# Optimization experiments

Hardware: AMD Instinct MI355X
Metric: run time of the kernel (lower is better)

The kernel has to match this reference:

```python
import jax, jax.numpy as jnp
import numpy as np

H = 256   # lstm2 hidden size
D_IN = 512  # lstm2 input size (256 fed-back out + 256 audio)
BN_EPS = 1e-5


def _lstm_cell(x, h, c, Wih, Whh, bih, bhh):
    # torch gate order: i, f, g, o
    z = x @ Wih.T + h @ Whh.T + bih + bhh  # (B, 4H)
    i, f, g, o = jnp.split(z, 4, axis=-1)
    i = jax.nn.sigmoid(i)
    f = jax.nn.sigmoid(f)
    g = jnp.tanh(g)
    o = jax.nn.sigmoid(o)
    c = f * c + i * g
    h = o * jnp.tanh(c)
    return h, c


def setup_inputs() -> dict:
    key = jax.random.key(0)
    ks = jax.random.split(key, 16)
    B, T, L = 256, 512, 16
    s = 0.05
    inp = {
        "rt": jax.random.normal(ks[0], (B, H), jnp.float32),
        "audio": jax.random.normal(ks[1], (B, T, H), jnp.float32),
        "s_rt": jax.random.normal(ks[2], (B, L, H), jnp.float32),
        # lstm2 layer 0
        "W_ih_l0": jax.random.normal(ks[3], (4 * H, D_IN), jnp.float32) * s,
        "W_hh_l0": jax.random.normal(ks[4], (4 * H, H), jnp.float32) * s,
        "b_ih_l0": jax.random.normal(ks[5], (4 * H,), jnp.float32) * s,
        "b_hh_l0": jax.random.normal(ks[6], (4 * H,), jnp.float32) * s,
        # lstm2 layer 1
        "W_ih_l1": jax.random.normal(ks[7], (4 * H, H), jnp.float32) * s,
        "W_hh_l1": jax.random.normal(ks[8], (4 * H, H), jnp.float32) * s,
        "b_ih_l1": jax.random.normal(ks[9], (4 * H,), jnp.float32) * s,
        "b_hh_l1": jax.random.normal(ks[10], (4 * H,), jnp.float32) * s,
        # rt_linear head: Linear(256,128) -> BN(128) -> ReLU -> Linear(128,6)
        "W1": jax.random.normal(ks[11], (128, H), jnp.float32) * s,
        "b1": jax.random.normal(ks[12], (128,), jnp.float32) * s,
        "gamma": jnp.ones((128,), jnp.float32),
        "beta": jnp.zeros((128,), jnp.float32),
        "W2": jax.random.normal(ks[13], (6, 128), jnp.float32) * s,
        "b2": jax.random.normal(ks[14], (6,), jnp.float32) * s,
        "max_len": 0,
    }
    return inp


def reference(rt, audio, s_rt,
              W_ih_l0, W_hh_l0, b_ih_l0, b_hh_l0,
              W_ih_l1, W_hh_l1, b_ih_l1, b_hh_l1,
              W1, b1, gamma, beta, W2, b2, max_len):
    B, T, _ = audio.shape
    prev_out = jnp.mean(s_rt, axis=1)  # (B, 256): torch.mean(s_rt, dim=1)
    h1 = c1 = h2 = c2 = jnp.zeros((B, H), audio.dtype)

    def step(carry, a_t):
        prev_out, h1, c1, h2, c2 = carry
        x = jnp.concatenate([prev_out, a_t], axis=-1)  # (B, 512)
        h1n, c1n = _lstm_cell(x, h1, c1, W_ih_l0, W_hh_l0, b_ih_l0, b_hh_l0)
        h2n, c2n = _lstm_cell(h1n, h2, c2, W_ih_l1, W_hh_l1, b_ih_l1, b_hh_l1)
        return (h2n, h1n, c1n, h2n, c2n), h2n

    audio_tm = jnp.transpose(audio, (1, 0, 2))  # (T, B, 256) time-major
    _, out_tm = jax.lax.scan(step, (prev_out, h1, c1, h2, c2), audio_tm)
    out = jnp.transpose(out_tm, (1, 0, 2)).reshape(-1, H)  # (B*T, 256)

    # rt_linear head, BatchNorm1d in training mode (batch stats)
    y = out @ W1.T + b1  # (B*T, 128)
    mu = jnp.mean(y, axis=0)
    var = jnp.var(y, axis=0)
    y = (y - mu) * jax.lax.rsqrt(var + BN_EPS) * gamma + beta
    y = jax.nn.relu(y)
    y = y @ W2.T + b2  # (B*T, 6)
    return y.reshape(B, T, -1)
```

## Files before the change

### kernel.cpp

```cpp
#include <hip/hip_runtime.h>
#include <stdint.h>

typedef unsigned int u32;
typedef unsigned short u16;
typedef unsigned long long u64;
typedef _Float16 f16;
typedef _Float16 h2_t __attribute__((ext_vector_type(2)));
typedef _Float16 f16x4 __attribute__((ext_vector_type(4)));
typedef _Float16 f16x8 __attribute__((ext_vector_type(8)));
typedef float f32x4 __attribute__((ext_vector_type(4)));
typedef float f32x16 __attribute__((ext_vector_type(16)));

#define TT 512
#define NF 128
#define NTOT (256 * TT)

#define OFF_WA0   0u
#define OFF_WA1   1572864u
#define OFF_WAH   2621440u
#define OFF_GSUM  2883584u
#define OFF_GSQ   2884096u
#define OFF_CTR   2884608u
#define OFF_GH1   2886656u
#define OFF_GH2   3017728u
#define OFF_Y     3148800u

__device__ __forceinline__ float sigf(float x) { return 1.0f / (1.0f + __expf(-x)); }
__device__ __forceinline__ float tanh_fast(float x) { return 1.0f - 2.0f / (__expf(2.0f * x) + 1.0f); }

__global__ void prep_kernel(const float* __restrict__ Wih0, const float* __restrict__ Whh0,
                            const float* __restrict__ Wih1, const float* __restrict__ Whh1,
                            const float* __restrict__ W1,
                            f16* __restrict__ WA0, f16* __restrict__ WA1, f16* __restrict__ WAH,
                            float* __restrict__ gz, u32* __restrict__ ctr) {
    int idx = blockIdx.x * 256 + threadIdx.x;
    const int n0 = 786432, n1 = 524288, n2 = 131072;
    if (idx < n0) {
        int u = idx >> 9, r9 = idx & 511;
        int lane = r9 >> 3, j = r9 & 7;
        int ks = u % 6; u /= 6;
        int wv = u & 7, w = u >> 3;
        int lr = lane & 31, h = lane >> 5;
        int r = ((lr >> 3) << 8) + 8 * w + (lr & 7);
        int seg = ks >> 1, sig = ks & 1;
        int c = 256 * seg + 32 * wv + 16 * sig + 8 * h + j;
        float v = (c < 512) ? Wih0[r * 512 + c] : Whh0[r * 256 + (c - 512)];
        WA0[idx] = (f16)v;
    } else if (idx < n0 + n1) {
        int i2 = idx - n0;
        int lane = (i2 >> 3) & 63, j = i2 & 7;
        int ks = (i2 >> 9) & 3, wv = (i2 >> 11) & 7, w = i2 >> 14;
        int lr = lane & 31, h = lane >> 5;
        int r = ((lr >> 3) << 8) + 8 * w + (lr & 7);
        int sig = ks & 1;
        int c = 32 * wv + 16 * sig + 8 * h + j;
        float v = (ks >> 1) ? Whh1[r * 256 + c] : Wih1[r * 256 + c];
        WA1[i2] = (f16)v;
    } else if (idx < n0 + n1 + n2) {
        int i2 = idx - n0 - n1;
        int u = i2 >> 9, r9 = i2 & 511;
        int lane = r9 >> 3, j = r9 & 7;
        int ks = u & 7, w = u >> 3;
        int m = lane & 15, hh = lane >> 4;
        int k = 32 * ks + 8 * hh + j;
        float v = (m < 4) ? W1[(4 * w + m) * 256 + k] : 0.f;
        WAH[i2] = (f16)v;
    } else if (idx < n0 + n1 + n2 + 256) {
        gz[idx - n0 - n1 - n2] = 0.f;
    } else if (idx < n0 + n1 + n2 + 256 + 512) {
        ctr[idx - n0 - n1 - n2 - 256] = 0u;
    }
}

#define MFMA32L(A, BP, C) (C) = __builtin_amdgcn_mfma_f32_32x32x16_f16( \
    __builtin_bit_cast(f16x8, (A)), __builtin_bit_cast(f16x8, *(const uint4*)(BP)), (C), 0, 0, 0)
#define MFMA32R(A, B, C) (C) = __builtin_amdgcn_mfma_f32_32x32x16_f16( \
    __builtin_bit_cast(f16x8, (A)), __builtin_bit_cast(f16x8, (B)), (C), 0, 0, 0)

#define ZZWR(KW, C) do { \
    f32x4 v0_ = {(C)[0], (C)[1], (C)[2], (C)[3]};    *(f32x4*)&zz[KW][n32][4 * h32] = v0_; \
    f32x4 v1_ = {(C)[4], (C)[5], (C)[6], (C)[7]};    *(f32x4*)&zz[KW][n32][8 + 4 * h32] = v1_; \
    f32x4 v2_ = {(C)[8], (C)[9], (C)[10], (C)[11]};  *(f32x4*)&zz[KW][n32][16 + 4 * h32] = v2_; \
    f32x4 v3_ = {(C)[12], (C)[13], (C)[14], (C)[15]}; *(f32x4*)&zz[KW][n32][24 + 4 * h32] = v3_; } while (0)

__global__ __launch_bounds__(512) void lstm_group_kernel(
    const float* __restrict__ audio, const float* __restrict__ s_rt,
    const uint4* __restrict__ WA0, const uint4* __restrict__ WA1, const uint4* __restrict__ WAH,
    const float* __restrict__ bih0, const float* __restrict__ bhh0,
    const float* __restrict__ bih1, const float* __restrict__ bhh1,
    const float* __restrict__ b1, u32* __restrict__ ctr,
    u64* __restrict__ gh1u, u64* __restrict__ gh2u,
    f16* __restrict__ ybuf, float* __restrict__ gsum, float* __restrict__ gsq)
{
    __shared__ f16 Xa[32][264];
    __shared__ f16 Xh2[32][264];
    __shared__ float zz[8][32][36];
    __shared__ f16 hst[32][8];
    __shared__ float bc0s[32], bc1s[32], b1s[4];
    __shared__ float pad_[2700];

    const int tid = threadIdx.x;
    const int w = blockIdx.x >> 3;
    const int g = blockIdx.x & 7;
    const int wv = tid >> 6;
    const int lane = tid & 63;
    const int n32 = lane & 31;
    const int h32 = (lane >> 5) & 1;
    const int ct = tid - 256;
    const int cb = ct >> 3, cj = ct & 7;

    if (tid == 0) { volatile float* vp = pad_; vp[0] = 0.f; }

    u32* const ctr1 = ctr + (g * 2 + 0) * 32;
    u32* const ctr2 = ctr + (g * 2 + 1) * 32;
    u64* const src1 = gh1u + (size_t)g * 2048;
    u64* const src2 = gh2u + (size_t)g * 2048;
    const size_t gbase = (size_t)n32 * 64 + 8 * wv + 2 * h32;

    uint4 a0[6], a1[4], ah[8] = {};
    #pragma unroll
    for (int ks = 0; ks < 6; ++ks) a0[ks] = WA0[((w * 8 + wv) * 6 + ks) * 64 + lane];
    #pragma unroll
    for (int ks = 0; ks < 4; ++ks) a1[ks] = WA1[((w * 8 + wv) * 4 + ks) * 64 + lane];
    if (wv < 2) {
        #pragma unroll
        for (int ks = 0; ks < 8; ++ks) ah[ks] = WAH[(w * 8 + ks) * 64 + lane];
    }

    if (tid < 32) {
        int r = ((tid >> 3) << 8) + 8 * w + (tid & 7);
        bc0s[tid] = bih0[r] + bhh0[r];
        bc1s[tid] = bih1[r] + bhh1[r];
    }
    if (tid < 4) b1s[tid] = b1[4 * w + tid];

    for (int it = tid; it < 32 * 256; it += 512) {
        int b = it >> 8, c = it & 255;
        const float* sp = s_rt + ((size_t)(32 * g + b) * 16) * 256 + c;
        float s = 0.f;
        #pragma unroll
        for (int l = 0; l < 16; ++l) s += sp[l * 256];
        Xh2[b][c] = (f16)(s * 0.0625f);
        Xa[b][c] = (f16)audio[((size_t)(32 * g + b) * 512) * 256 + c];
    }
    __syncthreads();

    uint4 f20 = *(const uint4*)&Xh2[n32][32 * wv + 8 * h32];
    uint4 f21 = *(const uint4*)&Xh2[n32][32 * wv + 16 + 8 * h32];
    uint4 f10 = {0, 0, 0, 0}, f11 = {0, 0, 0, 0};
    f32x16 aAcc = {};
    MFMA32L(a0[2], &Xa[n32][32 * wv + 8 * h32], aAcc);
    MFMA32L(a0[3], &Xa[n32][32 * wv + 16 + 8 * h32], aAcc);

    float c1 = 0.f, c2 = 0.f;
    float ys0 = 0, ys1 = 0, ys2 = 0, ys3 = 0, yq0 = 0, yq1 = 0, yq2 = 0, yq3 = 0;

    for (int t = 0; t < TT; ++t) {
        const u32 T = (u32)(t + 1);
        float4 av0, av1, av2, av3;
        if (t + 1 < TT) {
            const float4* a4 = (const float4*)audio;
            int b0 = tid >> 6, q0 = tid & 63;
            size_t base = ((size_t)(t + 1)) * 64 + q0;
            av0 = a4[(size_t)(32 * g + b0) * 32768 + base];
            av1 = a4[(size_t)(32 * g + b0 + 8) * 32768 + base];
            av2 = a4[(size_t)(32 * g + b0 + 16) * 32768 + base];
            av3 = a4[(size_t)(32 * g + b0 + 24) * 32768 + base];
        }
        MFMA32R(a0[0], f20, aAcc);
        MFMA32R(a0[1], f21, aAcc);
        ZZWR(wv, aAcc);
        __syncthreads();
        if (tid >= 256) {
            float z0 = bc0s[cj], z1 = bc0s[8 + cj], z2 = bc0s[16 + cj], z3 = bc0s[24 + cj];
            #pragma unroll
            for (int kw = 0; kw < 8; ++kw) {
                z0 += zz[kw][cb][cj];      z1 += zz[kw][cb][8 + cj];
                z2 += zz[kw][cb][16 + cj]; z3 += zz[kw][cb][24 + cj];
            }
            float c = sigf(z1) * c1 + sigf(z0) * tanh_fast(z2);
            c1 = c;
            hst[cb][cj] = (f16)(sigf(z3) * tanh_fast(c));
        }
        __syncthreads();
        if (wv == 7)
            __hip_atomic_store(src1 + (size_t)(lane >> 1) * 64 + 2 * w + (lane & 1),
                               ((const u64*)hst)[lane],
                               __ATOMIC_RELAXED, __HIP_MEMORY_SCOPE_AGENT);
        f32x16 Dacc = {};
        if (t > 0) {
            MFMA32R(a1[2], f20, Dacc);
            MFMA32R(a1[3], f21, Dacc);
        }
        if (wv == 7) {
            asm volatile("s_waitcnt vmcnt(0)" ::: "memory");
            if (lane == 0) {
                __hip_atomic_fetch_add(ctr1, 1u, __ATOMIC_RELAXED, __HIP_MEMORY_SCOPE_AGENT);
                u32 tgt = 32u * T; int gu = 0;
                while (__hip_atomic_load(ctr1, __ATOMIC_RELAXED, __HIP_MEMORY_SCOPE_AGENT) < tgt
                       && ++gu < 100000000) { __builtin_amdgcn_s_sleep(1); }
            }
        }
        __syncthreads();
        {
            u64 q0 = __hip_atomic_load(src1 + gbase + 0, __ATOMIC_RELAXED, __HIP_MEMORY_SCOPE_AGENT);
            u64 q1 = __hip_atomic_load(src1 + gbase + 1, __ATOMIC_RELAXED, __HIP_MEMORY_SCOPE_AGENT);
            u64 q2 = __hip_atomic_load(src1 + gbase + 4, __ATOMIC_RELAXED, __HIP_MEMORY_SCOPE_AGENT);
            u64 q3 = __hip_atomic_load(src1 + gbase + 5, __ATOMIC_RELAXED, __HIP_MEMORY_SCOPE_AGENT);
            f10.x = (u32)q0; f10.y = (u32)(q0 >> 32); f10.z = (u32)q1; f10.w = (u32)(q1 >> 32);
            f11.x = (u32)q2; f11.y = (u32)(q2 >> 32); f11.z = (u32)q3; f11.w = (u32)(q3 >> 32);
        }
        MFMA32R(a1[0], f10, Dacc);
        MFMA32R(a1[1], f11, Dacc);
        ZZWR(wv, Dacc);
        __syncthreads();
        if (tid >= 256) {
            float z0 = bc1s[cj], z1 = bc1s[8 + cj], z2 = bc1s[16 + cj], z3 = bc1s[24 + cj];
            #pragma unroll
            for (int kw = 0; kw < 8; ++kw) {
                z0 += zz[kw][cb][cj];      z1 += zz[kw][cb][8 + cj];
                z2 += zz[kw][cb][16 + cj]; z3 += zz[kw][cb][24 + cj];
            }
            float c = sigf(z1) * c2 + sigf(z0) * tanh_fast(z2);
            c2 = c;
            hst[cb][cj] = (f16)(sigf(z3) * tanh_fast(c));
        }
        __syncthreads();
        if (wv == 7)
            __hip_atomic_store(src2 + (size_t)(lane >> 1) * 64 + 2 * w + (lane & 1),
                               ((const u64*)hst)[lane],
                               __ATOMIC_RELAXED, __HIP_MEMORY_SCOPE_AGENT);
        if (t + 1 < TT) {
            #define AST(AV, S) do { \
                int b_ = (tid >> 6) + 8 * (S); int q_ = tid & 63; \
                h2_t p0_; p0_.x = (f16)(AV).x; p0_.y = (f16)(AV).y; \
                h2_t p1_; p1_.x = (f16)(AV).z; p1_.y = (f16)(AV).w; \
                uint2 pv_; pv_.x = __builtin_bit_cast(u32, p0_); pv_.y = __builtin_bit_cast(u32, p1_); \
                *(uint2*)&Xa[b_][4 * q_] = pv_; } while (0)
            AST(av0, 0); AST(av1, 1); AST(av2, 2); AST(av3, 3);
        }
        __syncthreads();
        aAcc = (f32x16){};
        if (t + 1 < TT) {
            MFMA32L(a0[2], &Xa[n32][32 * wv + 8 * h32], aAcc);
            MFMA32L(a0[3], &Xa[n32][32 * wv + 16 + 8 * h32], aAcc);
            MFMA32R(a0[4], f10, aAcc);
            MFMA32R(a0[5], f11, aAcc);
        }
        if (wv == 7) {
            asm volatile("s_waitcnt vmcnt(0)" ::: "memory");
            if (lane == 0) {
                __hip_atomic_fetch_add(ctr2, 1u, __ATOMIC_RELAXED, __HIP_MEMORY_SCOPE_AGENT);
                u32 tgt = 32u * T; int gu = 0;
                while (__hip_atomic_load(ctr2, __ATOMIC_RELAXED, __HIP_MEMORY_SCOPE_AGENT) < tgt
                       && ++gu < 100000000) { __builtin_amdgcn_s_sleep(1); }
            }
        }
        __syncthreads();
        {
            u64 q0 = __hip_atomic_load(src2 + gbase + 0, __ATOMIC_RELAXED, __HIP_MEMORY_SCOPE_AGENT);
            u64 q1 = __hip_atomic_load(src2 + gbase + 1, __ATOMIC_RELAXED, __HIP_MEMORY_SCOPE_AGENT);
            u64 q2 = __hip_atomic_load(src2 + gbase + 4, __ATOMIC_RELAXED, __HIP_MEMORY_SCOPE_AGENT);
            u64 q3 = __hip_atomic_load(src2 + gbase + 5, __ATOMIC_RELAXED, __HIP_MEMORY_SCOPE_AGENT);
            f20.x = (u32)q0; f20.y = (u32)(q0 >> 32); f20.z = (u32)q1; f20.w = (u32)(q1 >> 32);
            f21.x = (u32)q2; f21.y = (u32)(q2 >> 32); f21.z = (u32)q3; f21.w = (u32)(q3 >> 32);
            *(uint4*)&Xh2[n32][32 * wv + 8 * h32] = f20;
            *(uint4*)&Xh2[n32][32 * wv + 16 + 8 * h32] = f21;
        }
        __syncthreads();
        if (wv < 2) {
            f32x4 C = {};
            #pragma unroll
            for (int ks = 0; ks < 8; ++ks)
                C = __builtin_amdgcn_mfma_f32_16x16x32_f16(
                    __builtin_bit_cast(f16x8, ah[ks]),
                    __builtin_bit_cast(f16x8,
                        *(const uint4*)&Xh2[wv * 16 + (lane & 15)][32 * ks + 8 * ((lane >> 4) & 3)]),
                    C, 0, 0, 0);
            if (lane < 16) {
                float y0 = C[0] + b1s[0], y1 = C[1] + b1s[1];
                float y2 = C[2] + b1s[2], y3 = C[3] + b1s[3];
                ys0 += y0; yq0 += y0 * y0; ys1 += y1; yq1 += y1 * y1;
                ys2 += y2; yq2 += y2 * y2; ys3 += y3; yq3 += y3 * y3;
                f16x4 yp; yp[0] = (f16)y0; yp[1] = (f16)y1; yp[2] = (f16)y2; yp[3] = (f16)y3;
                int b = wv * 16 + lane;
                ((u64*)ybuf)[((size_t)(g * 32 + b) * 512 + t) * 32 + w] = __builtin_bit_cast(u64, yp);
            }
        }
    }
    if (wv < 2 && lane < 16) {
        #pragma unroll
        for (int m = 8; m >= 1; m >>= 1) {
            ys0 += __shfl_xor(ys0, m, 64); ys1 += __shfl_xor(ys1, m, 64);
            ys2 += __shfl_xor(ys2, m, 64); ys3 += __shfl_xor(ys3, m, 64);
            yq0 += __shfl_xor(yq0, m, 64); yq1 += __shfl_xor(yq1, m, 64);
            yq2 += __shfl_xor(yq2, m, 64); yq3 += __shfl_xor(yq3, m, 64);
        }
        if (lane == 0) {
            atomicAdd(&gsum[4 * w + 0], ys0); atomicAdd(&gsum[4 * w + 1], ys1);
            atomicAdd(&gsum[4 * w + 2], ys2); atomicAdd(&gsum[4 * w + 3], ys3);
            atomicAdd(&gsq[4 * w + 0], yq0); atomicAdd(&gsq[4 * w + 1], yq1);
            atomicAdd(&gsq[4 * w + 2], yq2); atomicAdd(&gsq[4 * w + 3], yq3);
        }
    }
}

__global__ __launch_bounds__(256) void head_kernel(
    const f16* __restrict__ ybuf, const float* __restrict__ gsum, const float* __restrict__ gsq,
    const float* __restrict__ gamma, const float* __restrict__ beta,
    const float* __restrict__ W2, const float* __restrict__ b2,
    float* __restrict__ out)
{
    __shared__ float sc[NF], sh[NF], W2s[6 * NF], b2s[6];
    const int tid = threadIdx.x;
    if (tid < NF) {
        const float invN = 1.f / (float)NTOT;
        float mu = gsum[tid] * invN;
        float var = gsq[tid] * invN - mu * mu;
        float iv = rsqrtf(var + 1e-5f);
        float s = gamma[tid] * iv;
        sc[tid] = s;
        sh[tid] = beta[tid] - mu * s;
    }
    for (int i = tid; i < 6 * NF; i += 256) W2s[i] = W2[i];
    if (tid < 6) b2s[tid] = b2[tid];
    __syncthreads();

    size_t n = (size_t)blockIdx.x * 256 + tid;
    const h2_t* yr = (const h2_t*)(ybuf + n * NF);
    float a0 = b2s[0], a1 = b2s[1], a2 = b2s[2], a3 = b2s[3], a4 = b2s[4], a5 = b2s[5];
    #pragma unroll 8
    for (int p = 0; p < 64; ++p) {
        h2_t v = yr[p];
        int f0 = 2 * p, f1 = 2 * p + 1;
        float v0 = fmaxf(fmaf((float)v.x, sc[f0], sh[f0]), 0.f);
        float v1 = fmaxf(fmaf((float)v.y, sc[f1], sh[f1]), 0.f);
        a0 = fmaf(v0, W2s[0 * NF + f0], a0); a0 = fmaf(v1, W2s[0 * NF + f1], a0);
        a1 = fmaf(v0, W2s[1 * NF + f0], a1); a1 = fmaf(v1, W2s[1 * NF + f1], a1);
        a2 = fmaf(v0, W2s[2 * NF + f0], a2); a2 = fmaf(v1, W2s[2 * NF + f1], a2);
        a3 = fmaf(v0, W2s[3 * NF + f0], a3); a3 = fmaf(v1, W2s[3 * NF + f1], a3);
        a4 = fmaf(v0, W2s[4 * NF + f0], a4); a4 = fmaf(v1, W2s[4 * NF + f1], a4);
        a5 = fmaf(v0, W2s[5 * NF + f0], a5); a5 = fmaf(v1, W2s[5 * NF + f1], a5);
    }
    float* op = out + n * 6;
    op[0] = a0; op[1] = a1; op[2] = a2; op[3] = a3; op[4] = a4; op[5] = a5;
}

extern "C" void kernel_launch(void* const* d_in, const int* in_sizes, int n_in,
                              void* d_out, int out_size, void* d_ws, size_t ws_size,
                              hipStream_t stream) {
    const float* audio = (const float*)d_in[1];
    const float* s_rt  = (const float*)d_in[2];
    const float* Wih0  = (const float*)d_in[3];
    const float* Whh0  = (const float*)d_in[4];
    const float* bih0  = (const float*)d_in[5];
    const float* bhh0  = (const float*)d_in[6];
    const float* Wih1  = (const float*)d_in[7];
    const float* Whh1  = (const float*)d_in[8];
    const float* bih1  = (const float*)d_in[9];
    const float* bhh1  = (const float*)d_in[10];
    const float* W1    = (const float*)d_in[11];
    const float* b1    = (const float*)d_in[12];
    const float* gamma = (const float*)d_in[13];
    const float* beta  = (const float*)d_in[14];
    const float* W2    = (const float*)d_in[15];
    const float* b2    = (const float*)d_in[16];

    char* ws = (char*)d_ws;
    f16* WA0    = (f16*)(ws + OFF_WA0);
    f16* WA1    = (f16*)(ws + OFF_WA1);
    f16* WAH    = (f16*)(ws + OFF_WAH);
    float* gsum = (float*)(ws + OFF_GSUM);
    float* gsq  = (float*)(ws + OFF_GSQ);
    u32* ctrp   = (u32*)(ws + OFF_CTR);
    u64* gh1u   = (u64*)(ws + OFF_GH1);
    u64* gh2u   = (u64*)(ws + OFF_GH2);
    f16* ybuf   = (f16*)(ws + OFF_Y);
    float* out  = (float*)d_out;

    prep_kernel<<<5635, 256, 0, stream>>>(Wih0, Whh0, Wih1, Whh1, W1,
                                          WA0, WA1, WAH, gsum, ctrp);

    lstm_group_kernel<<<256, 512, 0, stream>>>(audio, s_rt,
                                               (const uint4*)WA0, (const uint4*)WA1, (const uint4*)WAH,
                                               bih0, bhh0, bih1, bhh1, b1, ctrp,
                                               gh1u, gh2u, ybuf, gsum, gsq);

    head_kernel<<<NTOT / 256, 256, 0, stream>>>(ybuf, gsum, gsq, gamma, beta, W2, b2, out);
}
```

Before: 3.690 ms.

## Defer head GEMM into next step, vectorize h exchange, spin without sleep

The per-step head matmul now runs one step late, inside the layer-1 wait window, so a trailing barrier per step goes away; the final step's head is done after the loop. The h-state publish and gather use 16-byte global stores and loads with sc0 sc1 cache bits through inline asm instead of paired 8-byte atomics. The audio prefetch moves after the layer-1 gather, and the spin-wait loops drop s_sleep. This targets barrier and latency overhead on the serial recurrence path, at the cost of busier polling and reliance on asm cache-coherence semantics.

```diff
diff --git a/kernel.cpp b/kernel.cpp
--- a/kernel.cpp
+++ b/kernel.cpp
@@ -10,6 +10,7 @@
 typedef _Float16 f16x8 __attribute__((ext_vector_type(8)));
 typedef float f32x4 __attribute__((ext_vector_type(4)));
 typedef float f32x16 __attribute__((ext_vector_type(16)));
+typedef u32 u32x4 __attribute__((ext_vector_type(4)));
 
 #define TT 512
 #define NF 128
@@ -83,6 +84,34 @@
     f32x4 v2_ = {(C)[8], (C)[9], (C)[10], (C)[11]};  *(f32x4*)&zz[KW][n32][16 + 4 * h32] = v2_; \
     f32x4 v3_ = {(C)[12], (C)[13], (C)[14], (C)[15]}; *(f32x4*)&zz[KW][n32][24 + 4 * h32] = v3_; } while (0)
 
+#define GATHER2(F0, F1, P0, P1) asm volatile( \
+    "global_load_dwordx4 %0, %2, off sc0 sc1\n\t" \
+    "global_load_dwordx4 %1, %3, off sc0 sc1\n\t" \
+    "s_waitcnt vmcnt(0)" \
+    : "=&v"(F0), "=&v"(F1) : "v"(P0), "v"(P1) : "memory")
+
+#define PUBX4(PTR, DATA) asm volatile( \
+    "global_store_dwordx4 %0, %1, off sc0 sc1" :: "v"(PTR), "v"(DATA) : "memory")
+
+#define HEAD_BODY(TIDX) do { \
+    f32x4 C_ = {}; \
+    _Pragma("unroll") \
+    for (int ks_ = 0; ks_ < 8; ++ks_) \
+        C_ = __builtin_amdgcn_mfma_f32_16x16x32_f16( \
+            __builtin_bit_cast(f16x8, ah[ks_]), \
+            __builtin_bit_cast(f16x8, \
+                *(const uint4*)&Xh2[wv * 16 + (lane & 15)][32 * ks_ + 8 * ((lane >> 4) & 3)]), \
+            C_, 0, 0, 0); \
+    if (lane < 16) { \
+        float y0 = C_[0] + b1s[0], y1 = C_[1] + b1s[1]; \
+        float y2 = C_[2] + b1s[2], y3 = C_[3] + b1s[3]; \
+        ys0 += y0; yq0 += y0 * y0; ys1 += y1; yq1 += y1 * y1; \
+        ys2 += y2; yq2 += y2 * y2; ys3 += y3; yq3 += y3 * y3; \
+        f16x4 yp; yp[0] = (f16)y0; yp[1] = (f16)y1; yp[2] = (f16)y2; yp[3] = (f16)y3; \
+        int b_ = wv * 16 + lane; \
+        ((u64*)ybuf)[((size_t)(g * 32 + b_) * 512 + (TIDX)) * 32 + w] = __builtin_bit_cast(u64, yp); \
+    } } while (0)
+
 __global__ __launch_bounds__(512) void lstm_group_kernel(
     const float* __restrict__ audio, const float* __restrict__ s_rt,
     const uint4* __restrict__ WA0, const uint4* __restrict__ WA1, const uint4* __restrict__ WAH,
@@ -92,10 +121,10 @@
     u64* __restrict__ gh1u, u64* __restrict__ gh2u,
     f16* __restrict__ ybuf, float* __restrict__ gsum, float* __restrict__ gsq)
 {
-    __shared__ f16 Xa[32][264];
-    __shared__ f16 Xh2[32][264];
+    __shared__ __align__(16) f16 Xa[32][264];
+    __shared__ __align__(16) f16 Xh2[32][264];
     __shared__ float zz[8][32][36];
-    __shared__ f16 hst[32][8];
+    __shared__ __align__(16) f16 hst[32][8];
     __shared__ float bc0s[32], bc1s[32], b1s[4];
     __shared__ float pad_[2700];
 
@@ -145,9 +174,9 @@
     }
     __syncthreads();
 
-    uint4 f20 = *(const uint4*)&Xh2[n32][32 * wv + 8 * h32];
-    uint4 f21 = *(const uint4*)&Xh2[n32][32 * wv + 16 + 8 * h32];
-    uint4 f10 = {0, 0, 0, 0}, f11 = {0, 0, 0, 0};
+    u32x4 f20 = *(const u32x4*)&Xh2[n32][32 * wv + 8 * h32];
+    u32x4 f21 = *(const u32x4*)&Xh2[n32][32 * wv + 16 + 8 * h32];
+    u32x4 f10 = {0, 0, 0, 0}, f11 = {0, 0, 0, 0};
     f32x16 aAcc = {};
     MFMA32L(a0[2], &Xa[n32][32 * wv + 8 * h32], aAcc);
     MFMA32L(a0[3], &Xa[n32][32 * wv + 16 + 8 * h32], aAcc);
@@ -157,16 +186,6 @@
 
     for (int t = 0; t < TT; ++t) {
         const u32 T = (u32)(t + 1);
-        float4 av0, av1, av2, av3;
-        if (t + 1 < TT) {
-            const float4* a4 = (const float4*)audio;
-            int b0 = tid >> 6, q0 = tid & 63;
-            size_t base = ((size_t)(t + 1)) * 64 + q0;
-            av0 = a4[(size_t)(32 * g + b0) * 32768 + base];
-            av1 = a4[(size_t)(32 * g + b0 + 8) * 32768 + base];
-            av2 = a4[(size_t)(32 * g + b0 + 16) * 32768 + base];
-            av3 = a4[(size_t)(32 * g + b0 + 24) * 32768 + base];
-        }
         MFMA32R(a0[0], f20, aAcc);
         MFMA32R(a0[1], f21, aAcc);
         ZZWR(wv, aAcc);
@@ -183,32 +202,36 @@
             hst[cb][cj] = (f16)(sigf(z3) * tanh_fast(c));
         }
         __syncthreads();
-        if (wv == 7)
-            __hip_atomic_store(src1 + (size_t)(lane >> 1) * 64 + 2 * w + (lane & 1),
-                               ((const u64*)hst)[lane],
-                               __ATOMIC_RELAXED, __HIP_MEMORY_SCOPE_AGENT);
+        if (wv == 7 && lane < 32) {
+            u32x4 hv = *((const u32x4*)hst + lane);
+            PUBX4((void*)(src1 + (size_t)lane * 64 + 2 * w), hv);
+        }
         f32x16 Dacc = {};
         if (t > 0) {
             MFMA32R(a1[2], f20, Dacc);
             MFMA32R(a1[3], f21, Dacc);
         }
+        if (wv < 2 && t > 0) HEAD_BODY(t - 1);
         if (wv == 7) {
             asm volatile("s_waitcnt vmcnt(0)" ::: "memory");
             if (lane == 0) {
                 __hip_atomic_fetch_add(ctr1, 1u, __ATOMIC_RELAXED, __HIP_MEMORY_SCOPE_AGENT);
                 u32 tgt = 32u * T; int gu = 0;
                 while (__hip_atomic_load(ctr1, __ATOMIC_RELAXED, __HIP_MEMORY_SCOPE_AGENT) < tgt
-                       && ++gu < 100000000) { __builtin_amdgcn_s_sleep(1); }
+                       && ++gu < 100000000) { }
             }
         }
         __syncthreads();
-        {
-            u64 q0 = __hip_atomic_load(src1 + gbase + 0, __ATOMIC_RELAXED, __HIP_MEMORY_SCOPE_AGENT);
-            u64 q1 = __hip_atomic_load(src1 + gbase + 1, __ATOMIC_RELAXED, __HIP_MEMORY_SCOPE_AGENT);
-            u64 q2 = __hip_atomic_load(src1 + gbase + 4, __ATOMIC_RELAXED, __HIP_MEMORY_SCOPE_AGENT);
-            u64 q3 = __hip_atomic_load(src1 + gbase + 5, __ATOMIC_RELAXED, __HIP_MEMORY_SCOPE_AGENT);
-            f10.x = (u32)q0; f10.y = (u32)(q0 >> 32); f10.z = (u32)q1; f10.w = (u32)(q1 >> 32);
-            f11.x = (u32)q2; f11.y = (u32)(q2 >> 32); f11.z = (u32)q3; f11.w = (u32)(q3 >> 32);
+        GATHER2(f10, f11, (const void*)(src1 + gbase), (const void*)(src1 + gbase + 4));
+        float4 av0, av1, av2, av3;
+        if (t + 1 < TT) {
+            const float4* a4 = (const float4*)audio;
+            int b0 = tid >> 6, q0 = tid & 63;
+            size_t base = ((size_t)(t + 1)) * 64 + q0;
+            av0 = a4[(size_t)(32 * g + b0) * 32768 + base];
+            av1 = a4[(size_t)(32 * g + b0 + 8) * 32768 + base];
+            av2 = a4[(size_t)(32 * g + b0 + 16) * 32768 + base];
+            av3 = a4[(size_t)(32 * g + b0 + 24) * 32768 + base];
         }
         MFMA32R(a1[0], f10, Dacc);
         MFMA32R(a1[1], f11, Dacc);
@@ -226,10 +249,10 @@
             hst[cb][cj] = (f16)(sigf(z3) * tanh_fast(c));
         }
         __syncthreads();
-        if (wv == 7)
-            __hip_atomic_store(src2 + (size_t)(lane >> 1) * 64 + 2 * w + (lane & 1),
-                               ((const u64*)hst)[lane],
-                               __ATOMIC_RELAXED, __HIP_MEMORY_SCOPE_AGENT);
+        if (wv == 7 && lane < 32) {
+            u32x4 hv = *((const u32x4*)hst + lane);
+            PUBX4((void*)(src2 + (size_t)lane * 64 + 2 * w), hv);
+        }
         if (t + 1 < TT) {
             #define AST(AV, S) do { \
                 int b_ = (tid >> 6) + 8 * (S); int q_ = tid & 63; \
@@ -253,41 +276,16 @@
                 __hip_atomic_fetch_add(ctr2, 1u, __ATOMIC_RELAXED, __HIP_MEMORY_SCOPE_AGENT);
                 u32 tgt = 32u * T; int gu = 0;
                 while (__hip_atomic_load(ctr2, __ATOMIC_RELAXED, __HIP_MEMORY_SCOPE_AGENT) < tgt
-                       && ++gu < 100000000) { __builtin_amdgcn_s_sleep(1); }
+                       && ++gu < 100000000) { }
             }
         }
         __syncthreads();
-        {
-            u64 q0 = __hip_atomic_load(src2 + gbase + 0, __ATOMIC_RELAXED, __HIP_MEMORY_SCOPE_AGENT);
-            u64 q1 = __hip_atomic_load(src2 + gbase + 1, __ATOMIC_RELAXED, __HIP_MEMORY_SCOPE_AGENT);
-            u64 q2 = __hip_atomic_load(src2 + gbase + 4, __ATOMIC_RELAXED, __HIP_MEMORY_SCOPE_AGENT);
-            u64 q3 = __hip_atomic_load(src2 + gbase + 5, __ATOMIC_RELAXED, __HIP_MEMORY_SCOPE_AGENT);
-            f20.x = (u32)q0; f20.y = (u32)(q0 >> 32); f20.z = (u32)q1; f20.w = (u32)(q1 >> 32);
-            f21.x = (u32)q2; f21.y = (u32)(q2 >> 32); f21.z = (u32)q3; f21.w = (u32)(q3 >> 32);
-            *(uint4*)&Xh2[n32][32 * wv + 8 * h32] = f20;
-            *(uint4*)&Xh2[n32][32 * wv + 16 + 8 * h32] = f21;
-        }
-        __syncthreads();
-        if (wv < 2) {
-            f32x4 C = {};
-            #pragma unroll
-            for (int ks = 0; ks < 8; ++ks)
-                C = __builtin_amdgcn_mfma_f32_16x16x32_f16(
-                    __builtin_bit_cast(f16x8, ah[ks]),
-                    __builtin_bit_cast(f16x8,
-                        *(const uint4*)&Xh2[wv * 16 + (lane & 15)][32 * ks + 8 * ((lane >> 4) & 3)]),
-                    C, 0, 0, 0);
-            if (lane < 16) {
-                float y0 = C[0] + b1s[0], y1 = C[1] + b1s[1];
-                float y2 = C[2] + b1s[2], y3 = C[3] + b1s[3];
-                ys0 += y0; yq0 += y0 * y0; ys1 += y1; yq1 += y1 * y1;
-                ys2 += y2; yq2 += y2 * y2; ys3 += y3; yq3 += y3 * y3;
-                f16x4 yp; yp[0] = (f16)y0; yp[1] = (f16)y1; yp[2] = (f16)y2; yp[3] = (f16)y3;
-                int b = wv * 16 + lane;
-                ((u64*)ybuf)[((size_t)(g * 32 + b) * 512 + t) * 32 + w] = __builtin_bit_cast(u64, yp);
-            }
-        }
-    }
+        GATHER2(f20, f21, (const void*)(src2 + gbase), (const void*)(src2 + gbase + 4));
+        *(u32x4*)&Xh2[n32][32 * wv + 8 * h32] = f20;
+        *(u32x4*)&Xh2[n32][32 * wv + 16 + 8 * h32] = f21;
+    }
+    __syncthreads();
+    if (wv < 2) HEAD_BODY(TT - 1);
     if (wv < 2 && lane < 16) {
         #pragma unroll
         for (int m = 8; m >= 1; m >>= 1) {
```

After: 3.314 ms. 1.11x faster.
